# Optimization experiments

Hardware: AMD Instinct MI355X
Metric: run time of the kernel (lower is better)

Reference implementation:

```python
import jax, jax.numpy as jnp
import numpy as np

B, D, E, H, L = 16384, 512, 16, 256, 64
NOISE_EPS = 0.01


def setup_inputs() -> dict:
    key = jax.random.key(0)
    ks = jax.random.split(key, 8)
    s = 0.05
    return {
        "x": jax.random.normal(ks[0], (B, D), dtype=jnp.float32),
        "noise": jax.random.normal(ks[1], (B, E), dtype=jnp.float32),
        "w_gate": jax.random.normal(ks[2], (D, E), dtype=jnp.float32) * s,
        "w_noise": jax.random.normal(ks[3], (D, E), dtype=jnp.float32) * s,
        "W1": jax.random.normal(ks[4], (E, D, H), dtype=jnp.float32) * s,
        "b1": jnp.zeros((E, H), dtype=jnp.float32),
        "W2": jax.random.normal(ks[5], (E, H, L), dtype=jnp.float32) * s,
        "b2": jnp.zeros((E, L), dtype=jnp.float32),
    }


def _noisy_gating(x, noise, w_gate, w_noise):
    clean_logits = x @ w_gate                                   # [B, E]
    noise_stddev = jax.nn.softplus(x @ w_noise) + NOISE_EPS     # [B, E]
    logits = jax.nn.softmax(clean_logits + noise * noise_stddev, axis=1)
    mean_weight = jnp.mean(logits, axis=-1) - 1e-8              # [B]
    gates = jnp.where(logits >= mean_weight[:, None], logits, 0.0)
    gates = gates / jnp.sum(gates, axis=-1, keepdims=True)
    return gates


def reference(x, noise, w_gate, w_noise, W1, b1, W2, b2):
    gates = _noisy_gating(x, noise, w_gate, w_noise)            # [B, E]
    # Dense equivalent of SparseDispatcher dispatch -> expert MLP -> combine:
    # combine scatters expert_e(x[b]) * gates[b,e] into slot (b, e), zeros elsewhere;
    # since gates==0 at masked slots, this equals gates[:,:,None] * all-expert outputs.
    h = jnp.tanh(jnp.einsum("bd,edh->beh", x, W1) + b1[None])   # [B, E, H]
    y = jnp.einsum("beh,ehl->bel", h, W2) + b2[None]            # [B, E, L]
    return gates[:, :, None] * y                                # [B, E, L]
```

## Files before the change

### kernel.cpp

```cpp
#include <hip/hip_runtime.h>
#include <stdint.h>

#define BROWS 16384
#define DDIM  512
#define EEXP  16
#define HDIM  256
#define LDIM  64
#define BM    128

typedef __bf16  bf16x8  __attribute__((ext_vector_type(8)));
typedef float   floatx4 __attribute__((ext_vector_type(4)));
typedef ushort  ushort8 __attribute__((ext_vector_type(8)));
typedef unsigned int u32;

__device__ __forceinline__ ushort f2bf(float f) {
    uint32_t u = __builtin_bit_cast(uint32_t, f);
    u += 0x7fffu + ((u >> 16) & 1u);
    return (ushort)(u >> 16);
}

__device__ __forceinline__ float fast_tanh(float x) {
    float e = __builtin_amdgcn_exp2f(x * 2.8853900817779268f);
    return 1.0f - 2.0f * __builtin_amdgcn_rcpf(e + 1.0f);
}

__device__ __forceinline__ void gl_lds16(const void* g, void* l) {
    __builtin_amdgcn_global_load_lds(
        (const __attribute__((address_space(1))) u32*)g,
        (__attribute__((address_space(3))) u32*)l, 16, 0, 0);
}

__global__ __launch_bounds__(64) void init_cnt(u32* __restrict__ cnt) {
    if (threadIdx.x < EEXP) cnt[threadIdx.x] = 0;
}

__global__ __launch_bounds__(256) void gating_kernel(
    const float* __restrict__ x,
    const float* __restrict__ noise,
    const float* __restrict__ wg,
    const float* __restrict__ wn,
    float* __restrict__ gates,
    ushort* __restrict__ xbf,
    u32* __restrict__ cnt,
    u32* __restrict__ rowlist)
{
    __shared__ __align__(16) float xs[32 * 132];
    __shared__ __align__(16) float wTg[16 * 132];
    __shared__ __align__(16) float wTn[16 * 132];
    __shared__ u32 lcnt[16];
    __shared__ u32 gbase[16];
    __shared__ ushort lrows[16 * 32];

    const int t    = threadIdx.x;
    const int row0 = blockIdx.x * 32;
    const int og   = t & 15, rg = t >> 4;

    if (t < 16) lcnt[t] = 0;

    floatx4 accg4[2] = {}, accn4[2] = {};

    for (int ch = 0; ch < 4; ++ch) {
        const int k0 = ch * 128;
        __syncthreads();
        {
            int r = t >> 3, c = (t & 7) * 16;
            const float* src = &x[(size_t)(row0 + r) * DDIM + k0 + c];
            float4 f[4];
            #pragma unroll
            for (int i = 0; i < 4; ++i)
                f[i] = reinterpret_cast<const float4*>(src)[i];
            float* dst = &xs[r * 132 + c];
            #pragma unroll
            for (int i = 0; i < 4; ++i)
                reinterpret_cast<float4*>(dst)[i] = f[i];

            const int row = row0 + r;
            const int sw  = r & 7;
            #pragma unroll
            for (int i = 0; i < 2; ++i) {
                int cb = k0 + c + i * 8;
                int kb = cb >> 6;
                int g  = (cb >> 3) & 7;
                int gp = g ^ sw;
                float4 a = f[i * 2], b = f[i * 2 + 1];
                ushort8 t8;
                t8[0]=f2bf(a.x); t8[1]=f2bf(a.y); t8[2]=f2bf(a.z); t8[3]=f2bf(a.w);
                t8[4]=f2bf(b.x); t8[5]=f2bf(b.y); t8[6]=f2bf(b.z); t8[7]=f2bf(b.w);
                *reinterpret_cast<ushort8*>(&xbf[(size_t)row * DDIM + kb * 64 + gp * 8]) = t8;
            }
        }
        {
            int d = t >> 1, e0 = (t & 1) * 8;
            float4 a0 = *reinterpret_cast<const float4*>(&wg[(size_t)(k0 + d) * EEXP + e0]);
            float4 a1 = *reinterpret_cast<const float4*>(&wg[(size_t)(k0 + d) * EEXP + e0 + 4]);
            float4 b0 = *reinterpret_cast<const float4*>(&wn[(size_t)(k0 + d) * EEXP + e0]);
            float4 b1 = *reinterpret_cast<const float4*>(&wn[(size_t)(k0 + d) * EEXP + e0 + 4]);
            wTg[(e0+0)*132+d]=a0.x; wTg[(e0+1)*132+d]=a0.y; wTg[(e0+2)*132+d]=a0.z; wTg[(e0+3)*132+d]=a0.w;
            wTg[(e0+4)*132+d]=a1.x; wTg[(e0+5)*132+d]=a1.y; wTg[(e0+6)*132+d]=a1.z; wTg[(e0+7)*132+d]=a1.w;
            wTn[(e0+0)*132+d]=b0.x; wTn[(e0+1)*132+d]=b0.y; wTn[(e0+2)*132+d]=b0.z; wTn[(e0+3)*132+d]=b0.w;
            wTn[(e0+4)*132+d]=b1.x; wTn[(e0+5)*132+d]=b1.y; wTn[(e0+6)*132+d]=b1.z; wTn[(e0+7)*132+d]=b1.w;
        }
        __syncthreads();

        #pragma unroll 8
        for (int d4 = 0; d4 < 32; ++d4) {
            floatx4 wgv = *reinterpret_cast<const floatx4*>(&wTg[og * 132 + d4 * 4]);
            floatx4 wnv = *reinterpret_cast<const floatx4*>(&wTn[og * 132 + d4 * 4]);
            #pragma unroll
            for (int rr = 0; rr < 2; ++rr) {
                floatx4 xv = *reinterpret_cast<const floatx4*>(&xs[(rg * 2 + rr) * 132 + d4 * 4]);
                accg4[rr] += xv * wgv;
                accn4[rr] += xv * wnv;
            }
        }
    }

    #pragma unroll
    for (int rr = 0; rr < 2; ++rr) {
        const int row = row0 + rg * 2 + rr;
        float accg = accg4[rr][0] + accg4[rr][1] + accg4[rr][2] + accg4[rr][3];
        float accn = accn4[rr][0] + accn4[rr][1] + accn4[rr][2] + accn4[rr][3];

        float sp = fmaxf(accn, 0.f) + log1pf(expf(-fabsf(accn)));
        float stddev = sp + 0.01f;
        float nz = noise[(size_t)row * EEXP + og];
        float z = accg + nz * stddev;

        float m = z;
        #pragma unroll
        for (int mask = 8; mask >= 1; mask >>= 1)
            m = fmaxf(m, __shfl_xor(m, mask, 16));
        float ez = expf(z - m);
        float s = ez;
        #pragma unroll
        for (int mask = 8; mask >= 1; mask >>= 1)
            s += __shfl_xor(s, mask, 16);
        float logit = ez / s;

        float lsum = logit;
        #pragma unroll
        for (int mask = 8; mask >= 1; mask >>= 1)
            lsum += __shfl_xor(lsum, mask, 16);
        float mean = lsum * (1.0f / 16.0f) - 1e-8f;

        float gate = (logit >= mean) ? logit : 0.0f;
        float denom = gate;
        #pragma unroll
        for (int mask = 8; mask >= 1; mask >>= 1)
            denom += __shfl_xor(denom, mask, 16);

        gates[(size_t)row * EEXP + og] = gate / denom;

        if (gate > 0.0f) {
            u32 p = atomicAdd(&lcnt[og], 1u);
            lrows[og * 32 + p] = (ushort)(rg * 2 + rr);
        }
    }

    __syncthreads();
    if (t < 16) gbase[t] = atomicAdd(&cnt[t], lcnt[t]);
    __syncthreads();
    for (int i = t; i < 16 * 32; i += 256) {
        int e = i >> 5, j = i & 31;
        if ((u32)j < lcnt[e])
            rowlist[(size_t)e * BROWS + gbase[e] + j] = row0 + lrows[e * 32 + j];
    }
}

__global__ __launch_bounds__(256) void zero_fill(
    const float* __restrict__ gates, float* __restrict__ out)
{
    int i = blockIdx.x * 256 + threadIdx.x;
    int slot = i >> 4;
    if (gates[slot] == 0.0f) {
        float4 z = {0.f, 0.f, 0.f, 0.f};
        reinterpret_cast<float4*>(out)[i] = z;
    }
}

__global__ __launch_bounds__(256) void transpose_all(
    const float* __restrict__ W1, ushort* __restrict__ W1T,
    const float* __restrict__ W2, ushort* __restrict__ W2T)
{
    __shared__ float tile[32][33];
    int b = blockIdx.x;
    const float* src; ushort* dst; int R, C, c0, r0, swz, ei;
    if (b < 2048) {
        ei = b >> 7; int rem = b & 127;
        c0 = (rem & 7) * 32; r0 = (rem >> 3) * 32;
        R = DDIM; C = HDIM; swz = 1;
        src = W1; dst = W1T;
    } else {
        b -= 2048;
        ei = b >> 4; int rem = b & 15;
        c0 = (rem & 1) * 32; r0 = (rem >> 1) * 32;
        R = HDIM; C = LDIM; swz = 0;
        src = W2; dst = W2T;
    }
    const int tx = threadIdx.x & 31, ty = threadIdx.x >> 5;
    const float* s = src + (size_t)ei * R * C;
    ushort* d = dst + (size_t)ei * R * C;

    #pragma unroll
    for (int i = 0; i < 4; ++i) {
        int rr = ty + i * 8;
        tile[rr][tx] = s[(size_t)(r0 + rr) * C + c0 + tx];
    }
    __syncthreads();
    #pragma unroll
    for (int i = 0; i < 4; ++i) {
        int cc = ty + i * 8;
        int h = c0 + cc;
        int col = r0 + tx;
        int col2 = col;
        if (swz) {
            int g = (col >> 3) & 7;
            col2 = (col & ~63) | ((g ^ (h & 7)) << 3) | (col & 7);
        }
        d[(size_t)h * R + col2] = f2bf(tile[tx][cc]);
    }
}

__global__ __launch_bounds__(256, 2) void expert_kernel(
    const ushort* __restrict__ xbf,
    const float*  __restrict__ gates,
    const ushort* __restrict__ W1T,
    const float*  __restrict__ b1,
    const ushort* __restrict__ W2T,
    const float*  __restrict__ b2,
    const u32*    __restrict__ cnt,
    const u32*    __restrict__ rowlist,
    float* __restrict__ out)
{
    __shared__ __align__(16) ushort lds[32768];

    const int bx   = blockIdx.x;
    const int e    = bx & 15;
    const int t    = bx >> 4;

    const int count = (int)cnt[e];
    if (t * BM >= count) return;
    const int nrt = min(BM, count - t * BM);
    const u32* rl = rowlist + (size_t)e * BROWS + t * BM;

    const int tid  = threadIdx.x;
    const int lane = tid & 63;
    const int wave = tid >> 6;

    const int lr = lane & 15;
    const int q  = lane >> 4;
    const int kq = q * 8;
    const int rq = q * 4;
    const int la = lane >> 3, lb = lane & 7;

    const char* xg = (const char*)xbf;
    const char* w1 = (const char*)W1T + (size_t)e * HDIM * 1024;

    size_t abase[4]; int sxr[4];
    #pragma unroll
    for (int p = 0; p < 4; ++p) {
        int r  = wave * 32 + p * 8 + la;
        int rc = min(r, nrt - 1);
        u32 ri = rl[rc];
        abase[p] = (size_t)ri * 1024;
        sxr[p]   = (la ^ (int)(ri & 7)) << 4;
    }

    floatx4 acc[8][4] = {};

    for (int kb = 0; kb < 8; ++kb) {
        const int koff = kb * 128;
        #pragma unroll
        for (int p = 0; p < 4; ++p) {
            int c = wave * 4 + p;
            gl_lds16(xg + abase[p] + koff + ((lb << 4) ^ sxr[p]), &lds[c * 512]);
        }
        #pragma unroll
        for (int p = 0; p < 8; ++p) {
            int c = wave * 8 + p;
            gl_lds16(w1 + (size_t)(c * 8 + la) * 1024 + koff + (lb << 4), &lds[8192 + c * 512]);
        }
        __syncthreads();

        #pragma unroll
        for (int s = 0; s < 2; ++s) {
            const int g = s * 4 + q;
            bf16x8 af[8], bfr[4];
            #pragma unroll
            for (int i = 0; i < 8; ++i) {
                int r = i * 16 + lr;
                af[i] = *reinterpret_cast<const bf16x8*>(&lds[r * 64 + ((g ^ (r & 7)) << 3)]);
            }
            #pragma unroll
            for (int j = 0; j < 4; ++j) {
                int r = wave * 64 + j * 16 + lr;
                bfr[j] = *reinterpret_cast<const bf16x8*>(&lds[8192 + r * 64 + ((g ^ (r & 7)) << 3)]);
            }
            #pragma unroll
            for (int i = 0; i < 8; ++i)
                #pragma unroll
                for (int j = 0; j < 4; ++j)
                    acc[i][j] = __builtin_amdgcn_mfma_f32_16x16x32_bf16(
                        af[i], bfr[j], acc[i][j], 0, 0, 0);
        }
        __syncthreads();
    }

    float b1v[4];
    #pragma unroll
    for (int j = 0; j < 4; ++j)
        b1v[j] = b1[e * HDIM + wave * 64 + j * 16 + lr];

    #pragma unroll
    for (int i = 0; i < 8; ++i)
        #pragma unroll
        for (int j = 0; j < 4; ++j) {
            int c = wave * 64 + j * 16 + lr;
            int gg = c >> 3;
            #pragma unroll
            for (int rr = 0; rr < 4; ++rr) {
                int r = i * 16 + rq + rr;
                float v = fast_tanh(acc[i][j][rr] + b1v[j]);
                lds[r * 256 + (((gg & 24) | ((gg & 7) ^ (r & 7))) << 3) + (c & 7)] = f2bf(v);
            }
        }
    __syncthreads();

    const ushort* w2 = W2T + (size_t)e * LDIM * HDIM;
    floatx4 acc2[2][4] = {};
    #pragma unroll
    for (int s = 0; s < 8; ++s) {
        int g = s * 4 + q;
        bf16x8 af[2];
        #pragma unroll
        for (int it = 0; it < 2; ++it) {
            int r = wave * 32 + it * 16 + lr;
            af[it] = *reinterpret_cast<const bf16x8*>(
                &lds[r * 256 + (((g & 24) | ((g & 7) ^ (r & 7))) << 3)]);
        }
        #pragma unroll
        for (int j = 0; j < 4; ++j) {
            bf16x8 bfr = *reinterpret_cast<const bf16x8*>(
                &w2[(size_t)(j * 16 + lr) * HDIM + s * 32 + kq]);
            #pragma unroll
            for (int it = 0; it < 2; ++it)
                acc2[it][j] = __builtin_amdgcn_mfma_f32_16x16x32_bf16(
                    af[it], bfr, acc2[it][j], 0, 0, 0);
        }
    }

    float b2v[4];
    #pragma unroll
    for (int j = 0; j < 4; ++j)
        b2v[j] = b2[e * LDIM + j * 16 + lr];

    #pragma unroll
    for (int it = 0; it < 2; ++it)
        #pragma unroll
        for (int rr = 0; rr < 4; ++rr) {
            int r  = wave * 32 + it * 16 + rq + rr;
            int rc = min(r, nrt - 1);
            u32 ri = rl[rc];
            float gsc = gates[(size_t)ri * EEXP + e];
            if (r < nrt) {
                #pragma unroll
                for (int j = 0; j < 4; ++j)
                    out[(size_t)ri * (EEXP * LDIM) + e * LDIM + j * 16 + lr] =
                        (acc2[it][j][rr] + b2v[j]) * gsc;
            }
        }
}

extern "C" void kernel_launch(void* const* d_in, const int* in_sizes, int n_in,
                              void* d_out, int out_size, void* d_ws, size_t ws_size,
                              hipStream_t stream) {
    (void)in_sizes; (void)n_in; (void)out_size; (void)ws_size;
    const float* x     = (const float*)d_in[0];
    const float* noise = (const float*)d_in[1];
    const float* wg    = (const float*)d_in[2];
    const float* wn    = (const float*)d_in[3];
    const float* W1    = (const float*)d_in[4];
    const float* b1    = (const float*)d_in[5];
    const float* W2    = (const float*)d_in[6];
    const float* b2    = (const float*)d_in[7];
    float* out = (float*)d_out;

    char* ws = (char*)d_ws;
    float*  gates   = (float*)ws;
    ushort* W1T     = (ushort*)(ws + (1 << 20));
    ushort* W2T     = (ushort*)(ws + (5 << 20));
    ushort* xbf     = (ushort*)(ws + (6 << 20));
    u32*    cnt     = (u32*)(ws + (22 << 20));
    u32*    rowlist = (u32*)(ws + (22 << 20) + 4096);

    init_cnt<<<1, 64, 0, stream>>>(cnt);
    gating_kernel<<<BROWS / 32, 256, 0, stream>>>(x, noise, wg, wn, gates, xbf, cnt, rowlist);
    transpose_all<<<2048 + 256, 256, 0, stream>>>(W1, W1T, W2, W2T);
    zero_fill<<<(BROWS * EEXP * LDIM / 4) / 256, 256, 0, stream>>>(gates, out);
    expert_kernel<<<(BROWS / BM) * EEXP, 256, 0, stream>>>(
        xbf, gates, W1T, b1, W2T, b2, cnt, rowlist, out);
}
```

Measured before the change: 186.8 us.

## Deterministic two-pass row compaction, merge aux kernels, halve expert tile to BM=64

Replaces the atomic per-expert counter with per-block counts plus a separate compaction kernel that prefix-sums block counts, which removes the init_cnt launch and makes row order deterministic. Weight transpose and zero-fill are merged into one launch. The expert kernel tile drops from 128 to 64 rows with smaller LDS and a 4-blocks-per-CU launch bound, aiming for more occupancy and less tail waste. The cost is that W1 tiles are reloaded twice as often per row, plus one extra compaction launch.

```diff
diff --git a/kernel.cpp b/kernel.cpp
--- a/kernel.cpp
+++ b/kernel.cpp
@@ -6,7 +6,7 @@
 #define EEXP  16
 #define HDIM  256
 #define LDIM  64
-#define BM    128
+#define BM    64
 
 typedef __bf16  bf16x8  __attribute__((ext_vector_type(8)));
 typedef float   floatx4 __attribute__((ext_vector_type(4)));
@@ -28,10 +28,6 @@
     __builtin_amdgcn_global_load_lds(
         (const __attribute__((address_space(1))) u32*)g,
         (__attribute__((address_space(3))) u32*)l, 16, 0, 0);
-}
-
-__global__ __launch_bounds__(64) void init_cnt(u32* __restrict__ cnt) {
-    if (threadIdx.x < EEXP) cnt[threadIdx.x] = 0;
 }
 
 __global__ __launch_bounds__(256) void gating_kernel(
@@ -41,18 +37,18 @@
     const float* __restrict__ wn,
     float* __restrict__ gates,
     ushort* __restrict__ xbf,
-    u32* __restrict__ cnt,
-    u32* __restrict__ rowlist)
+    u32* __restrict__ cntb,
+    u32* __restrict__ rowtmp)
 {
     __shared__ __align__(16) float xs[32 * 132];
     __shared__ __align__(16) float wTg[16 * 132];
     __shared__ __align__(16) float wTn[16 * 132];
     __shared__ u32 lcnt[16];
-    __shared__ u32 gbase[16];
     __shared__ ushort lrows[16 * 32];
 
     const int t    = threadIdx.x;
-    const int row0 = blockIdx.x * 32;
+    const int blk  = blockIdx.x;
+    const int row0 = blk * 32;
     const int og   = t & 15, rg = t >> 4;
 
     if (t < 16) lcnt[t] = 0;
@@ -158,32 +154,62 @@
     }
 
     __syncthreads();
-    if (t < 16) gbase[t] = atomicAdd(&cnt[t], lcnt[t]);
-    __syncthreads();
+    if (t < 16) cntb[t * 512 + blk] = lcnt[t];
     for (int i = t; i < 16 * 32; i += 256) {
         int e = i >> 5, j = i & 31;
         if ((u32)j < lcnt[e])
-            rowlist[(size_t)e * BROWS + gbase[e] + j] = row0 + lrows[e * 32 + j];
-    }
-}
-
-__global__ __launch_bounds__(256) void zero_fill(
+            rowtmp[(size_t)e * 16384 + blk * 32 + j] = row0 + lrows[e * 32 + j];
+    }
+}
+
+__global__ __launch_bounds__(256) void compact_kernel(
+    const u32* __restrict__ cntb,
+    const u32* __restrict__ rowtmp,
+    u32* __restrict__ rowlist,
+    u32* __restrict__ cnt)
+{
+    __shared__ u32 base_s[16];
+    const int b    = blockIdx.x;
+    const int lane = threadIdx.x & 63;
+    const int wave = threadIdx.x >> 6;
+
+    for (int e = wave; e < 16; e += 4) {
+        u32 s = 0;
+        for (int i = lane; i < b; i += 64) s += cntb[e * 512 + i];
+        #pragma unroll
+        for (int off = 32; off; off >>= 1) s += __shfl_down(s, off, 64);
+        if (lane == 0) {
+            base_s[e] = s;
+            if (b == 511) cnt[e] = s + cntb[e * 512 + 511];
+        }
+    }
+    __syncthreads();
+
+    const int t = threadIdx.x;
+    for (int i = t; i < 512; i += 256) {
+        int e = i >> 5, j = i & 31;
+        if ((u32)j < cntb[e * 512 + b])
+            rowlist[(size_t)e * BROWS + base_s[e] + j] =
+                rowtmp[(size_t)e * 16384 + b * 32 + j];
+    }
+}
+
+__global__ __launch_bounds__(256) void aux_kernel(
+    const float* __restrict__ W1, ushort* __restrict__ W1T,
+    const float* __restrict__ W2, ushort* __restrict__ W2T,
     const float* __restrict__ gates, float* __restrict__ out)
 {
-    int i = blockIdx.x * 256 + threadIdx.x;
-    int slot = i >> 4;
-    if (gates[slot] == 0.0f) {
-        float4 z = {0.f, 0.f, 0.f, 0.f};
-        reinterpret_cast<float4*>(out)[i] = z;
-    }
-}
-
-__global__ __launch_bounds__(256) void transpose_all(
-    const float* __restrict__ W1, ushort* __restrict__ W1T,
-    const float* __restrict__ W2, ushort* __restrict__ W2T)
-{
+    int b = blockIdx.x;
+    if (b >= 2304) {
+        int i = (b - 2304) * 256 + threadIdx.x;
+        int slot = i >> 4;
+        if (gates[slot] == 0.0f) {
+            float4 z = {0.f, 0.f, 0.f, 0.f};
+            reinterpret_cast<float4*>(out)[i] = z;
+        }
+        return;
+    }
     __shared__ float tile[32][33];
-    int b = blockIdx.x;
     const float* src; ushort* dst; int R, C, c0, r0, swz, ei;
     if (b < 2048) {
         ei = b >> 7; int rem = b & 127;
@@ -221,7 +247,7 @@
     }
 }
 
-__global__ __launch_bounds__(256, 2) void expert_kernel(
+__global__ __launch_bounds__(256, 4) void expert_kernel(
     const ushort* __restrict__ xbf,
     const float*  __restrict__ gates,
     const ushort* __restrict__ W1T,
@@ -232,11 +258,11 @@
     const u32*    __restrict__ rowlist,
     float* __restrict__ out)
 {
-    __shared__ __align__(16) ushort lds[32768];
-
-    const int bx   = blockIdx.x;
-    const int e    = bx & 15;
-    const int t    = bx >> 4;
+    __shared__ __align__(16) ushort lds[20480];
+
+    const int bx = blockIdx.x;
+    const int e  = bx & 15;
+    const int t  = bx >> 4;
 
     const int count = (int)cnt[e];
     if (t * BM >= count) return;
@@ -256,48 +282,49 @@
     const char* xg = (const char*)xbf;
     const char* w1 = (const char*)W1T + (size_t)e * HDIM * 1024;
 
-    size_t abase[4]; int sxr[4];
-    #pragma unroll
-    for (int p = 0; p < 4; ++p) {
-        int r  = wave * 32 + p * 8 + la;
+    size_t abase[2]; int sxr[2];
+    #pragma unroll
+    for (int p = 0; p < 2; ++p) {
+        int r  = wave * 16 + p * 8 + la;
         int rc = min(r, nrt - 1);
         u32 ri = rl[rc];
         abase[p] = (size_t)ri * 1024;
         sxr[p]   = (la ^ (int)(ri & 7)) << 4;
     }
 
-    floatx4 acc[8][4] = {};
+    floatx4 acc[4][4] = {};
 
     for (int kb = 0; kb < 8; ++kb) {
         const int koff = kb * 128;
         #pragma unroll
-        for (int p = 0; p < 4; ++p) {
-            int c = wave * 4 + p;
+        for (int p = 0; p < 2; ++p) {
+            int c = wave * 2 + p;
             gl_lds16(xg + abase[p] + koff + ((lb << 4) ^ sxr[p]), &lds[c * 512]);
         }
         #pragma unroll
         for (int p = 0; p < 8; ++p) {
             int c = wave * 8 + p;
-            gl_lds16(w1 + (size_t)(c * 8 + la) * 1024 + koff + (lb << 4), &lds[8192 + c * 512]);
+            gl_lds16(w1 + (size_t)(c * 8 + la) * 1024 + koff + (lb << 4),
+                     &lds[4096 + c * 512]);
         }
         __syncthreads();
 
         #pragma unroll
         for (int s = 0; s < 2; ++s) {
             const int g = s * 4 + q;
-            bf16x8 af[8], bfr[4];
-            #pragma unroll
-            for (int i = 0; i < 8; ++i) {
+            bf16x8 af[4], bfr[4];
+            #pragma unroll
+            for (int i = 0; i < 4; ++i) {
                 int r = i * 16 + lr;
                 af[i] = *reinterpret_cast<const bf16x8*>(&lds[r * 64 + ((g ^ (r & 7)) << 3)]);
             }
             #pragma unroll
             for (int j = 0; j < 4; ++j) {
                 int r = wave * 64 + j * 16 + lr;
-                bfr[j] = *reinterpret_cast<const bf16x8*>(&lds[8192 + r * 64 + ((g ^ (r & 7)) << 3)]);
+                bfr[j] = *reinterpret_cast<const bf16x8*>(&lds[4096 + r * 64 + ((g ^ (r & 7)) << 3)]);
             }
             #pragma unroll
-            for (int i = 0; i < 8; ++i)
+            for (int i = 0; i < 4; ++i)
                 #pragma unroll
                 for (int j = 0; j < 4; ++j)
                     acc[i][j] = __builtin_amdgcn_mfma_f32_16x16x32_bf16(
@@ -312,7 +339,7 @@
         b1v[j] = b1[e * HDIM + wave * 64 + j * 16 + lr];
 
     #pragma unroll
-    for (int i = 0; i < 8; ++i)
+    for (int i = 0; i < 4; ++i)
         #pragma unroll
         for (int j = 0; j < 4; ++j) {
             int c = wave * 64 + j * 16 + lr;
@@ -327,25 +354,18 @@
     __syncthreads();
 
     const ushort* w2 = W2T + (size_t)e * LDIM * HDIM;
-    floatx4 acc2[2][4] = {};
+    floatx4 acc2[4] = {};
     #pragma unroll
     for (int s = 0; s < 8; ++s) {
+        int r = wave * 16 + lr;
         int g = s * 4 + q;
-        bf16x8 af[2];
-        #pragma unroll
-        for (int it = 0; it < 2; ++it) {
-            int r = wave * 32 + it * 16 + lr;
-            af[it] = *reinterpret_cast<const bf16x8*>(
-                &lds[r * 256 + (((g & 24) | ((g & 7) ^ (r & 7))) << 3)]);
-        }
+        bf16x8 af = *reinterpret_cast<const bf16x8*>(
+            &lds[r * 256 + (((g & 24) | ((g & 7) ^ (r & 7))) << 3)]);
         #pragma unroll
         for (int j = 0; j < 4; ++j) {
             bf16x8 bfr = *reinterpret_cast<const bf16x8*>(
                 &w2[(size_t)(j * 16 + lr) * HDIM + s * 32 + kq]);
-            #pragma unroll
-            for (int it = 0; it < 2; ++it)
-                acc2[it][j] = __builtin_amdgcn_mfma_f32_16x16x32_bf16(
-                    af[it], bfr, acc2[it][j], 0, 0, 0);
+            acc2[j] = __builtin_amdgcn_mfma_f32_16x16x32_bf16(af, bfr, acc2[j], 0, 0, 0);
         }
     }
 
@@ -355,20 +375,18 @@
         b2v[j] = b2[e * LDIM + j * 16 + lr];
 
     #pragma unroll
-    for (int it = 0; it < 2; ++it)
-        #pragma unroll
-        for (int rr = 0; rr < 4; ++rr) {
-            int r  = wave * 32 + it * 16 + rq + rr;
-            int rc = min(r, nrt - 1);
-            u32 ri = rl[rc];
-            float gsc = gates[(size_t)ri * EEXP + e];
-            if (r < nrt) {
-                #pragma unroll
-                for (int j = 0; j < 4; ++j)
-                    out[(size_t)ri * (EEXP * LDIM) + e * LDIM + j * 16 + lr] =
-                        (acc2[it][j][rr] + b2v[j]) * gsc;
-            }
-        }
+    for (int rr = 0; rr < 4; ++rr) {
+        int r  = wave * 16 + rq + rr;
+        int rc = min(r, nrt - 1);
+        u32 ri = rl[rc];
+        float gsc = gates[(size_t)ri * EEXP + e];
+        if (r < nrt) {
+            #pragma unroll
+            for (int j = 0; j < 4; ++j)
+                out[(size_t)ri * (EEXP * LDIM) + e * LDIM + j * 16 + lr] =
+                    (acc2[j][rr] + b2v[j]) * gsc;
+        }
+    }
 }
 
 extern "C" void kernel_launch(void* const* d_in, const int* in_sizes, int n_in,
@@ -390,13 +408,14 @@
     ushort* W1T     = (ushort*)(ws + (1 << 20));
     ushort* W2T     = (ushort*)(ws + (5 << 20));
     ushort* xbf     = (ushort*)(ws + (6 << 20));
-    u32*    cnt     = (u32*)(ws + (22 << 20));
-    u32*    rowlist = (u32*)(ws + (22 << 20) + 4096);
-
-    init_cnt<<<1, 64, 0, stream>>>(cnt);
-    gating_kernel<<<BROWS / 32, 256, 0, stream>>>(x, noise, wg, wn, gates, xbf, cnt, rowlist);
-    transpose_all<<<2048 + 256, 256, 0, stream>>>(W1, W1T, W2, W2T);
-    zero_fill<<<(BROWS * EEXP * LDIM / 4) / 256, 256, 0, stream>>>(gates, out);
+    u32*    cntb    = (u32*)(ws + (22 << 20));
+    u32*    cnt     = (u32*)(ws + (22 << 20) + (32 << 10));
+    u32*    rowtmp  = (u32*)(ws + (23 << 20));
+    u32*    rowlist = (u32*)(ws + (24 << 20));
+
+    gating_kernel<<<BROWS / 32, 256, 0, stream>>>(x, noise, wg, wn, gates, xbf, cntb, rowtmp);
+    compact_kernel<<<512, 256, 0, stream>>>(cntb, rowtmp, rowlist, cnt);
+    aux_kernel<<<2304 + 16384, 256, 0, stream>>>(W1, W1T, W2, W2T, gates, out);
     expert_kernel<<<(BROWS / BM) * EEXP, 256, 0, stream>>>(
         xbf, gates, W1T, b1, W2T, b2, cnt, rowlist, out);
 }
```

Measured after the change: 184.4 us. Within noise of the previous version (-1.3%).
